# Kernel optimization log

Hardware: AMD Instinct MI355X
Metric: run time of the kernel (lower is better)

## Reference

```python
import jax, jax.numpy as jnp
import numpy as np

B, P, K, L = 16, 1024, 20, 10  # clouds, points/cloud, knn k, cov rank l
NCLS = 40


def _jacobi3(A, iters=5):
    """Batched 3x3 symmetric eigendecomposition via cyclic Jacobi sweeps.
    Returns (eigvals (N,3), V (N,3,3)) with ROWS of V as eigenvectors,
    mimicking diag(cov, nr_iterations=5)."""
    N = A.shape[0]
    V = jnp.broadcast_to(jnp.eye(3, dtype=A.dtype), (N, 3, 3))
    for _ in range(iters):
        for (p, q) in ((0, 1), (0, 2), (1, 2)):
            app, aqq, apq = A[:, p, p], A[:, q, q], A[:, p, q]
            nz = jnp.abs(apq) > 1e-12
            denom = jnp.where(nz, 2.0 * apq, 1.0)
            tau = (aqq - app) / denom
            t = jnp.where(nz, jnp.sign(tau) / (jnp.abs(tau) + jnp.sqrt(1.0 + tau * tau)), 0.0)
            c = 1.0 / jnp.sqrt(1.0 + t * t)
            s = t * c
            G = jnp.broadcast_to(jnp.eye(3, dtype=A.dtype), (N, 3, 3))
            G = G.at[:, p, p].set(c).at[:, q, q].set(c).at[:, p, q].set(s).at[:, q, p].set(-s)
            A = jnp.einsum('nia,nik,nkb->nab', G, A, G)  # G^T A G
            V = jnp.einsum('nik,nkb->nib', V, G)          # V @ G (columns = eigvecs)
    S = jnp.diagonal(A, axis1=1, axis2=2)
    return S, jnp.swapaxes(V, 1, 2)  # rows = eigenvectors


def _knn_edges(pos):
    """k-NN within each cloud (no self loops). Returns (center, nbr) global idx, grouped per center."""
    pb = pos.reshape(B, P, 3)
    sq = jnp.sum(pb * pb, axis=-1)                             # (B,P)
    d2 = sq[:, :, None] + sq[:, None, :] - 2.0 * jnp.einsum('bpc,bqc->bpq', pb, pb)
    d2 = d2 + jnp.eye(P, dtype=pos.dtype)[None] * 1e10         # mask self
    _, idx = jax.lax.top_k(-d2, K)                             # (B,P,K) nearest
    offs = (jnp.arange(B, dtype=idx.dtype) * P)[:, None, None]
    nbr = (idx + offs).reshape(-1)                             # (B*P*K,)
    center = jnp.repeat(jnp.arange(B * P, dtype=idx.dtype), K)
    return center, nbr


def setup_inputs() -> dict:
    key = jax.random.key(0)
    ks = jax.random.split(key, 14)
    def lin(k, fi, fo):
        return jax.random.normal(k, (fi, fo), jnp.float32) / np.sqrt(fi)
    inp = {
        'pos': jax.random.normal(ks[0], (B * P, 3), jnp.float32),
        'W1': lin(ks[1], 3, 32),   'b1': jnp.zeros((32,), jnp.float32),
        'W2': lin(ks[2], 32, 15),  'b2': jnp.zeros((15,), jnp.float32),
        'W3': lin(ks[3], 18, 256), 'b3': jnp.zeros((256,), jnp.float32),
        'W4': lin(ks[4], 256, 256),'b4': jnp.zeros((256,), jnp.float32),
        'Wn1': lin(ks[5], 256, 256), 'bn1': jnp.zeros((256,), jnp.float32),
        'Wn2': lin(ks[6], 256, NCLS), 'bn2': jnp.zeros((NCLS,), jnp.float32),
        'batch': jnp.repeat(jnp.arange(B, dtype=jnp.int64), P),
    }
    return inp


def reference(pos, W1, b1, W2, b2, W3, b3, W4, b4, Wn1, bn1, Wn2, bn2, batch):
    N = B * P
    center, nbr = _knn_edges(pos)
    # per-point neighbor clusters (gather): (N, K, 3)
    clusters = pos[nbr].reshape(N, K, 3) - pos[:, None, :]
    # local covariance from first L neighbors + iterative eigendecomposition
    cov = jnp.einsum('nki,nkj->nij', clusters[:, :L], clusters[:, :L])
    _, V = _jacobi3(cov, iters=5)
    # reorient clusters: bmm(clusters, V^T)
    dir_clusters = jnp.einsum('nkj,nij->nki', clusters, V)
    signs = jnp.sign(jnp.sum(dir_clusters[:, :, 2], axis=1))
    dir_clusters = jnp.concatenate(
        [dir_clusters[:, :, :2], (dir_clusters[:, :, 2] * signs[:, None])[:, :, None]], axis=2)
    # DirectionalSplineConv3D (proxy): per-edge MLP on reoriented offsets, sum over k -> (N,15)
    h = jax.nn.relu(dir_clusters @ W1 + b1)
    feat = jax.nn.sigmoid(jnp.sum(h @ W2 + b2, axis=1))  # sigmoid as in SampleNetDD
    # DirectionalDense: gather neighbor features, rotate 3-groups, concat, per-edge MLP, sum
    cf = feat[nbr].reshape(N, K * 5, 3)                   # (E,15) -> (N, 5K, 3)
    dir_feat = jnp.einsum('nmj,nij->nmi', cf, V).reshape(N, K, 15)
    concat = jnp.concatenate([dir_clusters, dir_feat], axis=2)  # (N,K,18)
    h2 = jax.nn.relu(concat @ W3 + b3)
    h2 = jax.nn.relu(h2 @ W4 + b4)
    point_feat = jnp.sum(h2, axis=1)                      # (N,256)
    # mean-pool per cloud + head
    ys = point_feat.reshape(B, P, 256).mean(axis=1)
    y1 = jax.nn.elu(ys @ Wn1 + bn1)
    y2 = jax.nn.log_softmax(y1 @ Wn2 + bn2, axis=1)
    return y2
```

## Files before the change

### kernel.cpp

```cpp
#include <hip/hip_runtime.h>
#include <hip/hip_bf16.h>
#include <math.h>

#define NB   16
#define NP   1024
#define KN   20
#define LN   10
#define NPT  16384
#define NCLS 40

typedef short bf16x8 __attribute__((ext_vector_type(8)));
typedef float f32x4  __attribute__((ext_vector_type(4)));

__device__ __forceinline__ short f2bf(float x) {
    __hip_bfloat16 h = __float2bfloat16(x);
    return *reinterpret_cast<short*>(&h);
}
__device__ __forceinline__ float bf2f(short s) {
    unsigned u = ((unsigned)(unsigned short)s) << 16;
    return __uint_as_float(u);
}
__device__ __forceinline__ unsigned pack2bf(float lo, float hi) {
    return (unsigned)(unsigned short)f2bf(lo) | ((unsigned)(unsigned short)f2bf(hi) << 16);
}
__device__ __forceinline__ unsigned umn(unsigned a, unsigned b) { return a < b ? a : b; }
__device__ __forceinline__ unsigned umx(unsigned a, unsigned b) { return a < b ? b : a; }

__global__ __launch_bounds__(256) void prep_k(const float* __restrict__ W3,
                                              const float* __restrict__ W4,
                                              short* __restrict__ W3T,
                                              short* __restrict__ W4T)
{
    const int k = blockIdx.x;
    const int n = threadIdx.x;
    W4T[n * 256 + k] = f2bf(W4[k * 256 + n]);
    if (k < 32) {
        float v = (k < 18) ? W3[k * 256 + n] : 0.0f;
        W3T[n * 32 + k] = f2bf(v);
    }
}

__global__ __launch_bounds__(256, 2) void knn_k(const float* __restrict__ pos,
                                                int* __restrict__ nbr)
{
    __shared__ float4 sp[NP];
    const int t    = threadIdx.x;
    const int blk  = blockIdx.x;
    const int b    = blk >> 6;
    const int base = b * NP;

    for (int i = t; i < NP; i += 256) {
        float x = pos[(base + i) * 3 + 0];
        float y = pos[(base + i) * 3 + 1];
        float z = pos[(base + i) * 3 + 2];
        sp[i] = make_float4(x, y, z, x * x + y * y + z * z);
    }
    __syncthreads();

    const int s    = t & 15;
    const int cLoc = (blk & 63) * 16 + (t >> 4);
    const float4 cp = sp[cLoc];

    unsigned A[20];
#pragma unroll
    for (int k = 0; k < 20; ++k) A[k] = 0xFFFFFFFFu;

    const int q0 = s * 64;
    for (int ii = 0; ii < 64; ++ii) {
        int i = (ii + s) & 63;
        int q = q0 + i;
        float4 p = sp[q];
        float dot = cp.x * p.x + cp.y * p.y + cp.z * p.z;
        float d2  = (cp.w + p.w) - 2.0f * dot;
        unsigned u = __float_as_uint(d2);
        u ^= (unsigned)(((int)u >> 31) | 0x80000000);
        unsigned key = (u & 0xFFFFFC00u) | (unsigned)q;
        if (q == cLoc) key = 0xFFFFFFFFu;
        if (key < A[19]) {
            A[19] = key;
#pragma unroll
            for (int j = 19; j > 0; --j) {
                unsigned lo = umn(A[j], A[j - 1]), hi = umx(A[j], A[j - 1]);
                A[j - 1] = lo; A[j] = hi;
            }
        }
    }

#pragma unroll
    for (int m = 1; m <= 8; m <<= 1) {
        unsigned Bv[20];
#pragma unroll
        for (int k = 0; k < 20; ++k) Bv[k] = __shfl_xor(A[k], m);
        unsigned L[32];
#pragma unroll
        for (int i = 0; i < 12; ++i) L[i] = A[i];
#pragma unroll
        for (int i = 12; i < 20; ++i) L[i] = umn(A[i], Bv[31 - i]);
#pragma unroll
        for (int i = 20; i < 32; ++i) L[i] = Bv[31 - i];
#pragma unroll
        for (int d = 16; d >= 1; d >>= 1)
#pragma unroll
            for (int i = 0; i < 32; ++i)
                if ((i & d) == 0) {
                    unsigned lo = umn(L[i], L[i + d]), hi = umx(L[i], L[i + d]);
                    L[i] = lo; L[i + d] = hi;
                }
#pragma unroll
        for (int k = 0; k < 20; ++k) A[k] = L[k];
    }

    if (s == 0) {
        const int n = base + cLoc;
#pragma unroll
        for (int k = 0; k < 20; ++k)
            nbr[n * KN + k] = base + (int)(A[k] & 1023u);
    }
}

__device__ __forceinline__ void jrot(float& app, float& aqq, float& apq,
                                     float& apr, float& aqr,
                                     float& vp0, float& vp1, float& vp2,
                                     float& vq0, float& vq1, float& vq2)
{
    bool  nz    = fabsf(apq) > 1e-12f;
    float denom = nz ? 2.0f * apq : 1.0f;
    float tau   = (aqq - app) / denom;
    float sg    = (tau > 0.0f) ? 1.0f : ((tau < 0.0f) ? -1.0f : 0.0f);
    float t     = nz ? sg / (fabsf(tau) + sqrtf(1.0f + tau * tau)) : 0.0f;
    float c     = 1.0f / sqrtf(1.0f + t * t);
    float s     = t * c;

    float app_n = c * c * app - 2.0f * c * s * apq + s * s * aqq;
    float aqq_n = s * s * app + 2.0f * c * s * apq + c * c * aqq;
    float apq_n = c * s * (app - aqq) + (c * c - s * s) * apq;
    float apr_n = c * apr - s * aqr;
    float aqr_n = s * apr + c * aqr;
    app = app_n; aqq = aqq_n; apq = apq_n; apr = apr_n; aqr = aqr_n;

    float t0;
    t0 = c * vp0 - s * vq0; vq0 = s * vp0 + c * vq0; vp0 = t0;
    t0 = c * vp1 - s * vq1; vq1 = s * vp1 + c * vq1; vp1 = t0;
    t0 = c * vp2 - s * vq2; vq2 = s * vp2 + c * vq2; vp2 = t0;
}

__global__ __launch_bounds__(64) void geom_k(const float* __restrict__ pos,
                                             const int* __restrict__ nbr,
                                             const float* __restrict__ W1,
                                             const float* __restrict__ b1,
                                             const float* __restrict__ W2,
                                             const float* __restrict__ b2,
                                             float* __restrict__ dirc,
                                             short* __restrict__ featO,
                                             float* __restrict__ Vg)
{
    __shared__ float sW1[96], sb1[32], sb2[15], sW2[480];
    const int tid = threadIdx.x;
    for (int i = tid; i < 96;  i += 64) sW1[i] = W1[i];
    if (tid < 32) sb1[tid] = b1[tid];
    for (int i = tid; i < 480; i += 64) sW2[i] = W2[i];
    if (tid < 15) sb2[tid] = b2[tid];
    __syncthreads();

    const int n = blockIdx.x * 64 + tid;
    const float px = pos[n * 3 + 0], py = pos[n * 3 + 1], pz = pos[n * 3 + 2];

    float cl[KN][3];
#pragma unroll
    for (int k = 0; k < KN; ++k) {
        int j = nbr[n * KN + k];
        cl[k][0] = pos[j * 3 + 0] - px;
        cl[k][1] = pos[j * 3 + 1] - py;
        cl[k][2] = pos[j * 3 + 2] - pz;
    }

    float a00 = 0, a01 = 0, a02 = 0, a11 = 0, a12 = 0, a22 = 0;
#pragma unroll
    for (int k = 0; k < LN; ++k) {
        a00 += cl[k][0] * cl[k][0]; a01 += cl[k][0] * cl[k][1]; a02 += cl[k][0] * cl[k][2];
        a11 += cl[k][1] * cl[k][1]; a12 += cl[k][1] * cl[k][2]; a22 += cl[k][2] * cl[k][2];
    }

    float v00 = 1, v01 = 0, v02 = 0,
          v10 = 0, v11 = 1, v12 = 0,
          v20 = 0, v21 = 0, v22 = 1;
#pragma unroll
    for (int it = 0; it < 5; ++it) {
        jrot(a00, a11, a01, a02, a12, v00, v10, v20, v01, v11, v21);
        jrot(a00, a22, a02, a01, a12, v00, v10, v20, v02, v12, v22);
        jrot(a11, a22, a12, a01, a02, v01, v11, v21, v02, v12, v22);
    }

    float s2 = 0.0f;
#pragma unroll
    for (int k = 0; k < KN; ++k) {
        float d0 = cl[k][0] * v00 + cl[k][1] * v10 + cl[k][2] * v20;
        float d1 = cl[k][0] * v01 + cl[k][1] * v11 + cl[k][2] * v21;
        float d2 = cl[k][0] * v02 + cl[k][1] * v12 + cl[k][2] * v22;
        cl[k][0] = d0; cl[k][1] = d1; cl[k][2] = d2;
        s2 += d2;
    }
    float sg = (s2 > 0.0f) ? 1.0f : ((s2 < 0.0f) ? -1.0f : 0.0f);

#pragma unroll
    for (int k = 0; k < KN; ++k) {
        cl[k][2] *= sg;
        dirc[n * 60 + k * 3 + 0] = cl[k][0];
        dirc[n * 60 + k * 3 + 1] = cl[k][1];
        dirc[n * 60 + k * 3 + 2] = cl[k][2];
    }

    float hs[32];
#pragma unroll
    for (int c = 0; c < 32; ++c) {
        float w0 = sW1[c], w1 = sW1[32 + c], w2 = sW1[64 + c], bb = sb1[c];
        float acc = 0.0f;
#pragma unroll
        for (int k = 0; k < KN; ++k)
            acc += fmaxf(bb + cl[k][0] * w0 + cl[k][1] * w1 + cl[k][2] * w2, 0.0f);
        hs[c] = acc;
    }

    Vg[n * 9 + 0] = v00; Vg[n * 9 + 1] = v10; Vg[n * 9 + 2] = v20;
    Vg[n * 9 + 3] = v01; Vg[n * 9 + 4] = v11; Vg[n * 9 + 5] = v21;
    Vg[n * 9 + 6] = v02; Vg[n * 9 + 7] = v12; Vg[n * 9 + 8] = v22;

#pragma unroll
    for (int j = 0; j < 15; ++j) {
        float x = 20.0f * sb2[j];
#pragma unroll
        for (int c = 0; c < 32; ++c) x += hs[c] * sW2[c * 15 + j];
        featO[n * 15 + j] = f2bf(1.0f / (1.0f + expf(-x)));
    }
}

__global__ __launch_bounds__(256, 4) void mlp_k(const int* __restrict__ nbr,
                                                const float* __restrict__ dirc,
                                                const short* __restrict__ featB,
                                                const float* __restrict__ Vg,
                                                const short* __restrict__ W3T,
                                                const float* __restrict__ b3,
                                                const short* __restrict__ W4T,
                                                const float* __restrict__ b4,
                                                float* __restrict__ pf)
{
    __shared__ __align__(16) short H1L[64 * 256];
    __shared__ __align__(16) short concatL[64 * 40];
    __shared__ short sfeatS[60 * 16];
    __shared__ float Vr_s[27];

    const int t   = threadIdx.x;
    const int l   = t & 63;
    const int lg  = l >> 4;
    const int lc  = l & 15;
    const int n0w = (t >> 6) * 64;
    const int pt0 = blockIdx.x * 3;
    const int swz = (lc & 7) << 3;

    if (t >= 64 && t < 91) {
        int e = t - 64;
        int pt = pt0 + e / 9;
        Vr_s[e] = (pt < NPT) ? Vg[pt * 9 + (e % 9)] : 0.0f;
    }
    for (int i = t; i < 1280; i += 256) ((int*)concatL)[i] = 0;

    for (int i2 = t; i2 < 900; i2 += 256) {
        int nb = i2 / 15, c = i2 - nb * 15;
        int gi = pt0 * 20 + nb;
        int idx = (gi < NPT * 20) ? nbr[gi] : 0;
        sfeatS[nb * 16 + c] = featB[idx * 15 + c];
    }
    __syncthreads();

    for (int job = t; job < 1080; job += 256) {
        int p  = job / 360;
        int rr = job - p * 360;
        int k  = rr / 18;
        int c  = rr - k * 18;
        int pt = pt0 + p;
        float val = 0.0f;
        if (pt < NPT) {
            if (c < 3) {
                val = dirc[pt * 60 + k * 3 + c];
            } else {
                int e = c - 3, g = e / 3, i = e - g * 3;
                const short* fr = &sfeatS[(p * 20 + k) * 16 + g * 3];
                const float* Vr = Vr_s + p * 9;
                val = bf2f(fr[0]) * Vr[i * 3 + 0] + bf2f(fr[1]) * Vr[i * 3 + 1] + bf2f(fr[2]) * Vr[i * 3 + 2];
            }
        }
        concatL[(p * 20 + k) * 40 + c] = f2bf(val);
    }
    __syncthreads();

    {
        f32x4 accB[4][4];
#pragma unroll
        for (int mt = 0; mt < 4; ++mt)
#pragma unroll
            for (int nt = 0; nt < 4; ++nt)
#pragma unroll
                for (int r = 0; r < 4; ++r) accB[mt][nt][r] = 0.0f;

        bf16x8 aB[4], bB[4];
#pragma unroll
        for (int nt = 0; nt < 4; ++nt)
            aB[nt] = *(const bf16x8*)&concatL[(nt * 16 + lc) * 40 + lg * 8];
#pragma unroll
        for (int mt = 0; mt < 4; ++mt)
            bB[mt] = *(const bf16x8*)&W3T[(n0w + mt * 16 + lc) * 32 + lg * 8];
#pragma unroll
        for (int mt = 0; mt < 4; ++mt)
#pragma unroll
            for (int nt = 0; nt < 4; ++nt)
                accB[mt][nt] = __builtin_amdgcn_mfma_f32_16x16x32_bf16(bB[mt], aB[nt], accB[mt][nt], 0, 0, 0);

#pragma unroll
        for (int mt = 0; mt < 4; ++mt) {
            const int dim0 = n0w + mt * 16 + lg * 4;
            const float4 b3q = *(const float4*)&b3[dim0];
#pragma unroll
            for (int nt = 0; nt < 4; ++nt) {
                const int row = nt * 16 + lc;
                uint2 w;
                w.x = pack2bf(fmaxf(accB[mt][nt][0] + b3q.x, 0.0f),
                              fmaxf(accB[mt][nt][1] + b3q.y, 0.0f));
                w.y = pack2bf(fmaxf(accB[mt][nt][2] + b3q.z, 0.0f),
                              fmaxf(accB[mt][nt][3] + b3q.w, 0.0f));
                *reinterpret_cast<uint2*>(&H1L[row * 256 + (dim0 ^ swz)]) = w;
            }
        }
    }
    __syncthreads();

    f32x4 acc[4][4];
#pragma unroll
    for (int mt = 0; mt < 4; ++mt)
#pragma unroll
        for (int nt = 0; nt < 4; ++nt)
#pragma unroll
            for (int r = 0; r < 4; ++r) acc[mt][nt][r] = 0.0f;

#pragma unroll
    for (int ch = 0; ch < 8; ++ch) {
        bf16x8 a[4], b[4];
#pragma unroll
        for (int mt = 0; mt < 4; ++mt)
            a[mt] = *(const bf16x8*)&H1L[(mt * 16 + lc) * 256 + ((ch * 32 + lg * 8) ^ swz)];
#pragma unroll
        for (int nt = 0; nt < 4; ++nt)
            b[nt] = *(const bf16x8*)&W4T[(n0w + nt * 16 + lc) * 256 + ch * 32 + lg * 8];
#pragma unroll
        for (int mt = 0; mt < 4; ++mt)
#pragma unroll
            for (int nt = 0; nt < 4; ++nt)
                acc[mt][nt] = __builtin_amdgcn_mfma_f32_16x16x32_bf16(a[mt], b[nt], acc[mt][nt], 0, 0, 0);
    }

    const float m1 = (lg == 0) ? 1.0f : 0.0f;
    const float m2 = (lg <  2) ? 1.0f : 0.0f;
    const float m3 = (lg <  3) ? 1.0f : 0.0f;
    const int v0 = (pt0 + 0) < NPT, v1 = (pt0 + 1) < NPT, v2 = (pt0 + 2) < NPT;
#pragma unroll
    for (int nt = 0; nt < 4; ++nt) {
        int col = n0w + nt * 16 + lc;
        float b4v = b4[col];
        float a0 = 0.0f, a1 = 0.0f, a2 = 0.0f, a3 = 0.0f;
#pragma unroll
        for (int r = 0; r < 4; ++r) {
            a0 += fmaxf(acc[0][nt][r] + b4v, 0.0f);
            a1 += fmaxf(acc[1][nt][r] + b4v, 0.0f);
            a2 += fmaxf(acc[2][nt][r] + b4v, 0.0f);
            a3 += fmaxf(acc[3][nt][r] + b4v, 0.0f);
        }
        float s0 = a0 + m1 * a1;
        float s1 = (1.0f - m1) * a1 + m2 * a2;
        float s2 = (1.0f - m2) * a2 + m3 * a3;
        s0 += __shfl_xor(s0, 16); s0 += __shfl_xor(s0, 32);
        s1 += __shfl_xor(s1, 16); s1 += __shfl_xor(s1, 32);
        s2 += __shfl_xor(s2, 16); s2 += __shfl_xor(s2, 32);
        if (l < 16) {
            if (v0) pf[(pt0 + 0) * 256 + col] = s0;
            if (v1) pf[(pt0 + 1) * 256 + col] = s1;
            if (v2) pf[(pt0 + 2) * 256 + col] = s2;
        }
    }
}

__global__ __launch_bounds__(256) void psum_k(const float* __restrict__ pf,
                                              float* __restrict__ partial)
{
    const int t   = threadIdx.x;
    const int blk = blockIdx.x;
    const int b   = blk >> 5, sl = blk & 31;
    const float* basep = pf + ((size_t)b * NP + sl * 32) * 256 + t;
    float s = 0.0f;
#pragma unroll 8
    for (int p = 0; p < 32; ++p) s += basep[p * 256];
    partial[blk * 256 + t] = s;
}

__global__ __launch_bounds__(256) void head2_k(const float* __restrict__ partial,
                                               const float* __restrict__ Wn1,
                                               const float* __restrict__ bn1,
                                               const float* __restrict__ Wn2,
                                               const float* __restrict__ bn2,
                                               float* __restrict__ out)
{
    __shared__ float ysh[256], y1h[256], zsh[64];
    const int t = threadIdx.x, b = blockIdx.x;

    float s = 0.0f;
#pragma unroll
    for (int sl = 0; sl < 32; ++sl) s += partial[(b * 32 + sl) * 256 + t];
    ysh[t] = s * (1.0f / 1024.0f);
    __syncthreads();

    float acc = bn1[t];
    for (int c = 0; c < 256; ++c) acc += ysh[c] * Wn1[c * 256 + t];
    y1h[t] = (acc > 0.0f) ? acc : expm1f(acc);
    __syncthreads();

    if (t < NCLS) {
        float z = bn2[t];
        for (int c = 0; c < 256; ++c) z += y1h[c] * Wn2[c * NCLS + t];
        zsh[t] = z;
    }
    __syncthreads();

    if (t < 64) {
        float v = (t < NCLS) ? zsh[t] : -3.0e38f;
        float m = v;
#pragma unroll
        for (int off = 32; off >= 1; off >>= 1) m = fmaxf(m, __shfl_xor(m, off));
        float e = (t < NCLS) ? expf(zsh[t] - m) : 0.0f;
#pragma unroll
        for (int off = 32; off >= 1; off >>= 1) e += __shfl_xor(e, off);
        if (t < NCLS) out[b * NCLS + t] = zsh[t] - m - logf(e);
    }
}

extern "C" void kernel_launch(void* const* d_in, const int* in_sizes, int n_in,
                              void* d_out, int out_size, void* d_ws, size_t ws_size,
                              hipStream_t stream)
{
    const float* pos = (const float*)d_in[0];
    const float* W1  = (const float*)d_in[1];
    const float* b1  = (const float*)d_in[2];
    const float* W2  = (const float*)d_in[3];
    const float* b2  = (const float*)d_in[4];
    const float* W3  = (const float*)d_in[5];
    const float* b3  = (const float*)d_in[6];
    const float* W4  = (const float*)d_in[7];
    const float* b4  = (const float*)d_in[8];
    const float* Wn1 = (const float*)d_in[9];
    const float* bn1 = (const float*)d_in[10];
    const float* Wn2 = (const float*)d_in[11];
    const float* bn2 = (const float*)d_in[12];
    float* out = (float*)d_out;

    char* ws = (char*)d_ws;
    int*   nbr     = (int*)(ws + 0);
    float* dirc    = (float*)(ws + 1310720);
    short* feat    = (short*)(ws + 5242880);
    float* Vg      = (float*)(ws + 6225920);
    float* pf      = (float*)(ws + 6815744);
    short* W4T     = (short*)(ws + 23592960);
    short* W3T     = (short*)(ws + 23724032);
    float* partial = (float*)(ws + 5242880);

    prep_k <<<256,            256, 0, stream>>>(W3, W4, W3T, W4T);
    knn_k  <<<1024,           256, 0, stream>>>(pos, nbr);
    geom_k <<<256,             64, 0, stream>>>(pos, nbr, W1, b1, W2, b2, dirc, feat, Vg);
    mlp_k  <<<(NPT + 2) / 3,  256, 0, stream>>>(nbr, dirc, feat, Vg, W3T, b3, W4T, b4, pf);
    psum_k <<<512,            256, 0, stream>>>(pf, partial);
    head2_k<<<NB,             256, 0, stream>>>(partial, Wn1, bn1, Wn2, bn2, out);
}
```

Baseline: 311.3 us.

## Fuse weight prep, kNN and geometry kernels; pad features to 16 for vector loads

Merges prep_k, knn_k and geom_k into one launch. The geometry stage now runs in the kNN block using neighbour indices and positions already in shared memory, and extra blocks handle the weight transpose. The per-point feature rows are padded from 15 to 16 bf16 so mlp_k can gather them with 16-byte vector loads, and the workspace offsets are moved to match. The cost is that only 16 of 256 threads per block do the geometry work, serialising that phase after kNN inside each block.

```diff
diff --git a/kernel.cpp b/kernel.cpp
--- a/kernel.cpp
+++ b/kernel.cpp
@@ -26,26 +26,64 @@
 __device__ __forceinline__ unsigned umn(unsigned a, unsigned b) { return a < b ? a : b; }
 __device__ __forceinline__ unsigned umx(unsigned a, unsigned b) { return a < b ? b : a; }
 
-__global__ __launch_bounds__(256) void prep_k(const float* __restrict__ W3,
-                                              const float* __restrict__ W4,
-                                              short* __restrict__ W3T,
-                                              short* __restrict__ W4T)
-{
-    const int k = blockIdx.x;
-    const int n = threadIdx.x;
-    W4T[n * 256 + k] = f2bf(W4[k * 256 + n]);
-    if (k < 32) {
-        float v = (k < 18) ? W3[k * 256 + n] : 0.0f;
-        W3T[n * 32 + k] = f2bf(v);
-    }
-}
-
-__global__ __launch_bounds__(256, 2) void knn_k(const float* __restrict__ pos,
-                                                int* __restrict__ nbr)
-{
+__device__ __forceinline__ void jrot(float& app, float& aqq, float& apq,
+                                     float& apr, float& aqr,
+                                     float& vp0, float& vp1, float& vp2,
+                                     float& vq0, float& vq1, float& vq2)
+{
+    bool  nz    = fabsf(apq) > 1e-12f;
+    float denom = nz ? 2.0f * apq : 1.0f;
+    float tau   = (aqq - app) / denom;
+    float sg    = (tau > 0.0f) ? 1.0f : ((tau < 0.0f) ? -1.0f : 0.0f);
+    float t     = nz ? sg / (fabsf(tau) + sqrtf(1.0f + tau * tau)) : 0.0f;
+    float c     = 1.0f / sqrtf(1.0f + t * t);
+    float s     = t * c;
+
+    float app_n = c * c * app - 2.0f * c * s * apq + s * s * aqq;
+    float aqq_n = s * s * app + 2.0f * c * s * apq + c * c * aqq;
+    float apq_n = c * s * (app - aqq) + (c * c - s * s) * apq;
+    float apr_n = c * apr - s * aqr;
+    float aqr_n = s * apr + c * aqr;
+    app = app_n; aqq = aqq_n; apq = apq_n; apr = apr_n; aqr = aqr_n;
+
+    float t0;
+    t0 = c * vp0 - s * vq0; vq0 = s * vp0 + c * vq0; vp0 = t0;
+    t0 = c * vp1 - s * vq1; vq1 = s * vp1 + c * vq1; vp1 = t0;
+    t0 = c * vp2 - s * vq2; vq2 = s * vp2 + c * vq2; vp2 = t0;
+}
+
+__global__ __launch_bounds__(256, 2) void knng_k(const float* __restrict__ pos,
+                                                 const float* __restrict__ W3,
+                                                 const float* __restrict__ W4,
+                                                 short* __restrict__ W3T,
+                                                 short* __restrict__ W4T,
+                                                 const float* __restrict__ W1,
+                                                 const float* __restrict__ b1,
+                                                 const float* __restrict__ W2,
+                                                 const float* __restrict__ b2,
+                                                 int* __restrict__ nbr,
+                                                 float* __restrict__ dirc,
+                                                 short* __restrict__ featO,
+                                                 float* __restrict__ Vg)
+{
+    const int t   = threadIdx.x;
+    const int blk = blockIdx.x;
+
+    if (blk >= 1024) {
+        const int k = blk - 1024;
+        const int n = t;
+        W4T[n * 256 + k] = f2bf(W4[k * 256 + n]);
+        if (k < 32) {
+            float v = (k < 18) ? W3[k * 256 + n] : 0.0f;
+            W3T[n * 32 + k] = f2bf(v);
+        }
+        return;
+    }
+
     __shared__ float4 sp[NP];
-    const int t    = threadIdx.x;
-    const int blk  = blockIdx.x;
+    __shared__ int    nbrL[16][20];
+    __shared__ float  sW1[96], sb1[32], sb2[15], sW2[480];
+
     const int b    = blk >> 6;
     const int base = b * NP;
 
@@ -55,6 +93,10 @@
         float z = pos[(base + i) * 3 + 2];
         sp[i] = make_float4(x, y, z, x * x + y * y + z * z);
     }
+    if (t < 96)  sW1[t] = W1[t];
+    if (t >= 96 && t < 128) sb1[t - 96] = b1[t - 96];
+    if (t >= 128 && t < 143) sb2[t - 128] = b2[t - 128];
+    for (int i = t; i < 480; i += 256) sW2[i] = W2[i];
     __syncthreads();
 
     const int s    = t & 15;
@@ -112,125 +154,88 @@
 
     if (s == 0) {
         const int n = base + cLoc;
-#pragma unroll
-        for (int k = 0; k < 20; ++k)
-            nbr[n * KN + k] = base + (int)(A[k] & 1023u);
-    }
-}
-
-__device__ __forceinline__ void jrot(float& app, float& aqq, float& apq,
-                                     float& apr, float& aqr,
-                                     float& vp0, float& vp1, float& vp2,
-                                     float& vq0, float& vq1, float& vq2)
-{
-    bool  nz    = fabsf(apq) > 1e-12f;
-    float denom = nz ? 2.0f * apq : 1.0f;
-    float tau   = (aqq - app) / denom;
-    float sg    = (tau > 0.0f) ? 1.0f : ((tau < 0.0f) ? -1.0f : 0.0f);
-    float t     = nz ? sg / (fabsf(tau) + sqrtf(1.0f + tau * tau)) : 0.0f;
-    float c     = 1.0f / sqrtf(1.0f + t * t);
-    float s     = t * c;
-
-    float app_n = c * c * app - 2.0f * c * s * apq + s * s * aqq;
-    float aqq_n = s * s * app + 2.0f * c * s * apq + c * c * aqq;
-    float apq_n = c * s * (app - aqq) + (c * c - s * s) * apq;
-    float apr_n = c * apr - s * aqr;
-    float aqr_n = s * apr + c * aqr;
-    app = app_n; aqq = aqq_n; apq = apq_n; apr = apr_n; aqr = aqr_n;
-
-    float t0;
-    t0 = c * vp0 - s * vq0; vq0 = s * vp0 + c * vq0; vp0 = t0;
-    t0 = c * vp1 - s * vq1; vq1 = s * vp1 + c * vq1; vp1 = t0;
-    t0 = c * vp2 - s * vq2; vq2 = s * vp2 + c * vq2; vp2 = t0;
-}
-
-__global__ __launch_bounds__(64) void geom_k(const float* __restrict__ pos,
-                                             const int* __restrict__ nbr,
-                                             const float* __restrict__ W1,
-                                             const float* __restrict__ b1,
-                                             const float* __restrict__ W2,
-                                             const float* __restrict__ b2,
-                                             float* __restrict__ dirc,
-                                             short* __restrict__ featO,
-                                             float* __restrict__ Vg)
-{
-    __shared__ float sW1[96], sb1[32], sb2[15], sW2[480];
-    const int tid = threadIdx.x;
-    for (int i = tid; i < 96;  i += 64) sW1[i] = W1[i];
-    if (tid < 32) sb1[tid] = b1[tid];
-    for (int i = tid; i < 480; i += 64) sW2[i] = W2[i];
-    if (tid < 15) sb2[tid] = b2[tid];
-    __syncthreads();
-
-    const int n = blockIdx.x * 64 + tid;
-    const float px = pos[n * 3 + 0], py = pos[n * 3 + 1], pz = pos[n * 3 + 2];
-
-    float cl[KN][3];
-#pragma unroll
-    for (int k = 0; k < KN; ++k) {
-        int j = nbr[n * KN + k];
-        cl[k][0] = pos[j * 3 + 0] - px;
-        cl[k][1] = pos[j * 3 + 1] - py;
-        cl[k][2] = pos[j * 3 + 2] - pz;
-    }
-
-    float a00 = 0, a01 = 0, a02 = 0, a11 = 0, a12 = 0, a22 = 0;
-#pragma unroll
-    for (int k = 0; k < LN; ++k) {
-        a00 += cl[k][0] * cl[k][0]; a01 += cl[k][0] * cl[k][1]; a02 += cl[k][0] * cl[k][2];
-        a11 += cl[k][1] * cl[k][1]; a12 += cl[k][1] * cl[k][2]; a22 += cl[k][2] * cl[k][2];
-    }
-
-    float v00 = 1, v01 = 0, v02 = 0,
-          v10 = 0, v11 = 1, v12 = 0,
-          v20 = 0, v21 = 0, v22 = 1;
-#pragma unroll
-    for (int it = 0; it < 5; ++it) {
-        jrot(a00, a11, a01, a02, a12, v00, v10, v20, v01, v11, v21);
-        jrot(a00, a22, a02, a01, a12, v00, v10, v20, v02, v12, v22);
-        jrot(a11, a22, a12, a01, a02, v01, v11, v21, v02, v12, v22);
-    }
-
-    float s2 = 0.0f;
-#pragma unroll
-    for (int k = 0; k < KN; ++k) {
-        float d0 = cl[k][0] * v00 + cl[k][1] * v10 + cl[k][2] * v20;
-        float d1 = cl[k][0] * v01 + cl[k][1] * v11 + cl[k][2] * v21;
-        float d2 = cl[k][0] * v02 + cl[k][1] * v12 + cl[k][2] * v22;
-        cl[k][0] = d0; cl[k][1] = d1; cl[k][2] = d2;
-        s2 += d2;
-    }
-    float sg = (s2 > 0.0f) ? 1.0f : ((s2 < 0.0f) ? -1.0f : 0.0f);
-
-#pragma unroll
-    for (int k = 0; k < KN; ++k) {
-        cl[k][2] *= sg;
-        dirc[n * 60 + k * 3 + 0] = cl[k][0];
-        dirc[n * 60 + k * 3 + 1] = cl[k][1];
-        dirc[n * 60 + k * 3 + 2] = cl[k][2];
-    }
-
-    float hs[32];
-#pragma unroll
-    for (int c = 0; c < 32; ++c) {
-        float w0 = sW1[c], w1 = sW1[32 + c], w2 = sW1[64 + c], bb = sb1[c];
-        float acc = 0.0f;
-#pragma unroll
-        for (int k = 0; k < KN; ++k)
-            acc += fmaxf(bb + cl[k][0] * w0 + cl[k][1] * w1 + cl[k][2] * w2, 0.0f);
-        hs[c] = acc;
-    }
-
-    Vg[n * 9 + 0] = v00; Vg[n * 9 + 1] = v10; Vg[n * 9 + 2] = v20;
-    Vg[n * 9 + 3] = v01; Vg[n * 9 + 4] = v11; Vg[n * 9 + 5] = v21;
-    Vg[n * 9 + 6] = v02; Vg[n * 9 + 7] = v12; Vg[n * 9 + 8] = v22;
-
-#pragma unroll
-    for (int j = 0; j < 15; ++j) {
-        float x = 20.0f * sb2[j];
-#pragma unroll
-        for (int c = 0; c < 32; ++c) x += hs[c] * sW2[c * 15 + j];
-        featO[n * 15 + j] = f2bf(1.0f / (1.0f + expf(-x)));
+        const int c = t >> 4;
+#pragma unroll
+        for (int k = 0; k < 20; ++k) {
+            int loc = (int)(A[k] & 1023u);
+            nbrL[c][k] = loc;
+            nbr[n * KN + k] = base + loc;
+        }
+    }
+    __syncthreads();
+
+    if (t < 16) {
+        const int cl0 = (blk & 63) * 16 + t;
+        const int n   = base + cl0;
+        const float px = sp[cl0].x, py = sp[cl0].y, pz = sp[cl0].z;
+
+        float cl[KN][3];
+#pragma unroll
+        for (int k = 0; k < KN; ++k) {
+            int j = nbrL[t][k];
+            cl[k][0] = sp[j].x - px;
+            cl[k][1] = sp[j].y - py;
+            cl[k][2] = sp[j].z - pz;
+        }
+
+        float a00 = 0, a01 = 0, a02 = 0, a11 = 0, a12 = 0, a22 = 0;
+#pragma unroll
+        for (int k = 0; k < LN; ++k) {
+            a00 += cl[k][0] * cl[k][0]; a01 += cl[k][0] * cl[k][1]; a02 += cl[k][0] * cl[k][2];
+            a11 += cl[k][1] * cl[k][1]; a12 += cl[k][1] * cl[k][2]; a22 += cl[k][2] * cl[k][2];
+        }
+
+        float v00 = 1, v01 = 0, v02 = 0,
+              v10 = 0, v11 = 1, v12 = 0,
+              v20 = 0, v21 = 0, v22 = 1;
+#pragma unroll
+        for (int it = 0; it < 5; ++it) {
+            jrot(a00, a11, a01, a02, a12, v00, v10, v20, v01, v11, v21);
+            jrot(a00, a22, a02, a01, a12, v00, v10, v20, v02, v12, v22);
+            jrot(a11, a22, a12, a01, a02, v01, v11, v21, v02, v12, v22);
+        }
+
+        float s2 = 0.0f;
+#pragma unroll
+        for (int k = 0; k < KN; ++k) {
+            float d0 = cl[k][0] * v00 + cl[k][1] * v10 + cl[k][2] * v20;
+            float d1 = cl[k][0] * v01 + cl[k][1] * v11 + cl[k][2] * v21;
+            float d2 = cl[k][0] * v02 + cl[k][1] * v12 + cl[k][2] * v22;
+            cl[k][0] = d0; cl[k][1] = d1; cl[k][2] = d2;
+            s2 += d2;
+        }
+        float sg = (s2 > 0.0f) ? 1.0f : ((s2 < 0.0f) ? -1.0f : 0.0f);
+
+#pragma unroll
+        for (int k = 0; k < KN; ++k) {
+            cl[k][2] *= sg;
+            dirc[n * 60 + k * 3 + 0] = cl[k][0];
+            dirc[n * 60 + k * 3 + 1] = cl[k][1];
+            dirc[n * 60 + k * 3 + 2] = cl[k][2];
+        }
+
+        float hs[32];
+#pragma unroll
+        for (int c = 0; c < 32; ++c) {
+            float w0 = sW1[c], w1 = sW1[32 + c], w2 = sW1[64 + c], bb = sb1[c];
+            float acc = 0.0f;
+#pragma unroll
+            for (int k = 0; k < KN; ++k)
+                acc += fmaxf(bb + cl[k][0] * w0 + cl[k][1] * w1 + cl[k][2] * w2, 0.0f);
+            hs[c] = acc;
+        }
+
+        Vg[n * 9 + 0] = v00; Vg[n * 9 + 1] = v10; Vg[n * 9 + 2] = v20;
+        Vg[n * 9 + 3] = v01; Vg[n * 9 + 4] = v11; Vg[n * 9 + 5] = v21;
+        Vg[n * 9 + 6] = v02; Vg[n * 9 + 7] = v12; Vg[n * 9 + 8] = v22;
+
+#pragma unroll
+        for (int j = 0; j < 15; ++j) {
+            float x = 20.0f * sb2[j];
+#pragma unroll
+            for (int c = 0; c < 32; ++c) x += hs[c] * sW2[c * 15 + j];
+            featO[n * 16 + j] = f2bf(1.0f / (1.0f + expf(-x)));
+        }
     }
 }
 
@@ -246,7 +251,7 @@
 {
     __shared__ __align__(16) short H1L[64 * 256];
     __shared__ __align__(16) short concatL[64 * 40];
-    __shared__ short sfeatS[60 * 16];
+    __shared__ __align__(16) short sfeatS[60 * 16];
     __shared__ float Vr_s[27];
 
     const int t   = threadIdx.x;
@@ -264,11 +269,12 @@
     }
     for (int i = t; i < 1280; i += 256) ((int*)concatL)[i] = 0;
 
-    for (int i2 = t; i2 < 900; i2 += 256) {
-        int nb = i2 / 15, c = i2 - nb * 15;
+    if (t < 120) {
+        int nb = t >> 1, half = t & 1;
         int gi = pt0 * 20 + nb;
         int idx = (gi < NPT * 20) ? nbr[gi] : 0;
-        sfeatS[nb * 16 + c] = featB[idx * 15 + c];
+        *reinterpret_cast<uint4*>(&sfeatS[nb * 16 + half * 8]) =
+            *reinterpret_cast<const uint4*>(&featB[idx * 16 + half * 8]);
     }
     __syncthreads();
 
@@ -463,15 +469,14 @@
     int*   nbr     = (int*)(ws + 0);
     float* dirc    = (float*)(ws + 1310720);
     short* feat    = (short*)(ws + 5242880);
-    float* Vg      = (float*)(ws + 6225920);
-    float* pf      = (float*)(ws + 6815744);
-    short* W4T     = (short*)(ws + 23592960);
-    short* W3T     = (short*)(ws + 23724032);
-    float* partial = (float*)(ws + 5242880);
-
-    prep_k <<<256,            256, 0, stream>>>(W3, W4, W3T, W4T);
-    knn_k  <<<1024,           256, 0, stream>>>(pos, nbr);
-    geom_k <<<256,             64, 0, stream>>>(pos, nbr, W1, b1, W2, b2, dirc, feat, Vg);
+    float* Vg      = (float*)(ws + 5767168);
+    float* pf      = (float*)(ws + 6356992);
+    short* W4T     = (short*)(ws + 23134208);
+    short* W3T     = (short*)(ws + 23265280);
+    float* partial = (float*)(ws + 1310720);
+
+    knng_k <<<1280,           256, 0, stream>>>(pos, W3, W4, W3T, W4T,
+                                                W1, b1, W2, b2, nbr, dirc, feat, Vg);
     mlp_k  <<<(NPT + 2) / 3,  256, 0, stream>>>(nbr, dirc, feat, Vg, W3T, b3, W4T, b4, pf);
     psum_k <<<512,            256, 0, stream>>>(pf, partial);
     head2_k<<<NB,             256, 0, stream>>>(partial, Wn1, bn1, Wn2, bn2, out);
```

After: 488.8 us. +57.0%, slower.
